# Kernel tuning notes

Measured on AMD Instinct MI355X. Metric: run time of the kernel, lower is better.

The kernel has to match this reference:

```python
import jax, jax.numpy as jnp
import numpy as np

N_NODES = 50000


def _gcn_conv(x, src, dst, W, b, num_nodes):
    """PyG GCNConv: out = D^{-1/2}(A+I)D^{-1/2} (x @ W) + b, self-loops added."""
    h = x @ W  # [N, out]
    # degrees over edges incl. self-loops (src/dst already include self-loops)
    ones = jnp.ones(src.shape[0], dtype=h.dtype)
    deg = jax.ops.segment_sum(ones, dst, num_segments=num_nodes)
    dinv = jnp.where(deg > 0, jax.lax.rsqrt(deg), 0.0)
    norm = dinv[src] * dinv[dst]  # [E]
    msgs = h[src] * norm[:, None]  # [E, out] gather (memory-bound)
    out = jax.ops.segment_sum(msgs, dst, num_segments=num_nodes)
    return out + b


def setup_inputs() -> dict:
    key = jax.random.key(0)
    ks = jax.random.split(key, 8)
    in_c, h2, h1, out_c = 256, 256, 128, 128
    x = jax.random.normal(ks[0], (N_NODES, in_c), dtype=jnp.float32)
    edge_index = jax.random.randint(ks[1], (2, 800000), 0, N_NODES, dtype=jnp.int64)
    def glorot(k, fi, fo):
        s = float(np.sqrt(6.0 / (fi + fo)))
        return jax.random.uniform(k, (fi, fo), jnp.float32, -s, s)
    return {
        "x": x,
        "edge_index": edge_index,
        "W1": glorot(ks[2], in_c, h2), "b1": jnp.zeros((h2,), jnp.float32),
        "W2": glorot(ks[3], h2, h1), "b2": jnp.zeros((h1,), jnp.float32),
        "W3": glorot(ks[4], h1, out_c), "b3": jnp.zeros((out_c,), jnp.float32),
    }


def reference(x, edge_index, W1, b1, W2, b2, W3, b3):
    n = x.shape[0]
    loops = jnp.arange(n, dtype=edge_index.dtype)
    src = jnp.concatenate([edge_index[0], loops])
    dst = jnp.concatenate([edge_index[1], loops])
    # dropout is a no-op in eval mode (training=False)
    h1 = jax.nn.relu(_gcn_conv(x, src, dst, W1, b1, n))
    h2 = jax.nn.relu(_gcn_conv(h1, src, dst, W2, b2, n))
    h3 = jax.nn.relu(_gcn_conv(h2, src, dst, W3, b3, n))
    return jnp.concatenate([h1, h2, h3], axis=1)
```

## Files before the change

kernel.cpp:

```cpp
#include <hip/hip_runtime.h>

typedef __attribute__((ext_vector_type(8))) short bfrag8;
typedef __attribute__((ext_vector_type(4))) float f32x4v;

__device__ inline short f2bf(float f) {
    unsigned u = __builtin_bit_cast(unsigned, f);
    u = (u + 0x7FFFu + ((u >> 16) & 1u)) >> 16;
    return (short)u;
}
__device__ inline float bf2f(short s) {
    unsigned u = ((unsigned)(unsigned short)s) << 16;
    return __builtin_bit_cast(float, u);
}
__device__ inline int pack2(short lo, short hi) {
    return (int)(((unsigned)(unsigned short)lo) | (((unsigned)(unsigned short)hi) << 16));
}
__device__ inline int pad16i(int v) { return (v + 15) & ~15; }


__global__ void deg_count_kernel(const int* __restrict__ dst, int E, int* __restrict__ deg) {
    int e = blockIdx.x * blockDim.x + threadIdx.x;
    if (e < E) atomicAdd(&deg[dst[e]], 1);
}

__global__ void block_sum_kernel(const int* __restrict__ deg, int n, int* __restrict__ bsums) {
    int i = blockIdx.x * 256 + threadIdx.x;
    int v = (i < n) ? pad16i(deg[i] + 1) : 0;
#pragma unroll
    for (int off = 32; off > 0; off >>= 1) v += __shfl_down(v, off);
    __shared__ int wsum[4];
    int lane = threadIdx.x & 63, w = threadIdx.x >> 6;
    if (lane == 0) wsum[w] = v;
    __syncthreads();
    if (threadIdx.x == 0) bsums[blockIdx.x] = wsum[0] + wsum[1] + wsum[2] + wsum[3];
}

__global__ void scan_bsums_kernel(int* __restrict__ bsums, int B, int* __restrict__ offs, int n) {
    __shared__ int s[256];
    int tid = threadIdx.x;
    int v = (tid < B) ? bsums[tid] : 0;
    s[tid] = v;
    __syncthreads();
    for (int off = 1; off < 256; off <<= 1) {
        int t = (tid >= off) ? s[tid - off] : 0;
        __syncthreads();
        s[tid] += t;
        __syncthreads();
    }
    if (tid < B) bsums[tid] = (tid == 0) ? 0 : s[tid - 1];
    if (tid == 0) offs[n] = s[255];
}

__global__ void scan_final_kernel(const int* __restrict__ deg, int n,
                                  const int* __restrict__ bsums,
                                  int* __restrict__ offs, int* __restrict__ cursor,
                                  float* __restrict__ dinv, int* __restrict__ csr) {
    __shared__ int s[256];
    int tid = threadIdx.x;
    int i = blockIdx.x * 256 + tid;
    int vt = (i < n) ? deg[i] + 1 : 0;
    int pv = (i < n) ? pad16i(vt) : 0;
    s[tid] = pv;
    __syncthreads();
    for (int off = 1; off < 256; off <<= 1) {
        int t = (tid >= off) ? s[tid - off] : 0;
        __syncthreads();
        s[tid] += t;
        __syncthreads();
    }
    if (i < n) {
        int excl = s[tid] - pv + bsums[blockIdx.x];
        offs[i] = excl;
        csr[excl] = i;
        cursor[i] = excl + 1;
        for (int p = excl + vt; p < excl + pv; ++p) csr[p] = n;
        dinv[i] = rsqrtf((float)vt);
    } else {
        dinv[i] = 0.f;
    }
}

__global__ void csr_fill_kernel(const int* __restrict__ src, const int* __restrict__ dst, int E,
                                int* __restrict__ cursor, int* __restrict__ csr) {
    int e = blockIdx.x * blockDim.x + threadIdx.x;
    if (e < E) {
        int d = dst[e];
        int p = atomicAdd(&cursor[d], 1);
        csr[p] = src[e];
    }
}


__global__ void prep_w_kernel(const float* __restrict__ W1, short* __restrict__ Wt1,
                              const float* __restrict__ W2, short* __restrict__ Wt2,
                              const float* __restrict__ W3, short* __restrict__ Wt3) {
    int i = blockIdx.x * blockDim.x + threadIdx.x;
    if (i < 65536) {
        int k = i >> 8, n = i & 255;
        Wt1[n * 256 + k] = f2bf(W1[i]);
    } else if (i < 65536 + 32768) {
        int j = i - 65536;
        int k = j >> 7, n = j & 127;
        Wt2[n * 256 + k] = f2bf(W2[j]);
    } else {
        int j = i - 65536 - 32768;
        int k = j >> 7, n = j & 127;
        Wt3[n * 128 + k] = f2bf(W3[j]);
    }
}


__global__ void x2b_kernel(const float* __restrict__ x, short* __restrict__ xb,
                           int total8, int totalp8) {
    int i = blockIdx.x * blockDim.x + threadIdx.x;
    if (i < total8) {
        const float4* p = (const float4*)(x + (size_t)i * 8);
        float4 v0 = p[0], v1 = p[1];
        int4 w = make_int4(pack2(f2bf(v0.x), f2bf(v0.y)), pack2(f2bf(v0.z), f2bf(v0.w)),
                           pack2(f2bf(v1.x), f2bf(v1.y)), pack2(f2bf(v1.z), f2bf(v1.w)));
        *(int4*)(xb + (size_t)i * 8) = w;
    } else if (i < totalp8) {
        *(int4*)(xb + (size_t)i * 8) = make_int4(0, 0, 0, 0);
    }
}


template<int K>
__global__ __launch_bounds__(256, 2) void gemm_skinny_kernel(
        const short* __restrict__ A,
        const short* __restrict__ Bt,
        const float* __restrict__ dinv,
        short* __restrict__ Tout, int ldt) {
    constexpr int BSTR = K + 8;
    __shared__ short Bs[64 * BSTR];

    const int tid = threadIdx.x;
    const int lane = tid & 63;
    const int wid = tid >> 6;
    const int l15 = lane & 15;
    const int quad = lane >> 4;
    const int q8 = quad * 8;
    const int bn = blockIdx.y * 64;
    const int row0 = blockIdx.x * 256 + wid * 64;

    {
        constexpr int TOT16 = 64 * K / 8;
#pragma unroll
        for (int i = tid; i < TOT16; i += 256) {
            int r = i / (K / 8);
            int c = (i % (K / 8)) * 8;
            *(int4*)&Bs[r * BSTR + c] = *(const int4*)&Bt[(size_t)(bn + r) * K + c];
        }
    }
    __syncthreads();

    f32x4v acc[4][4];
#pragma unroll
    for (int i = 0; i < 4; ++i)
#pragma unroll
        for (int j = 0; j < 4; ++j) acc[i][j] = (f32x4v){0.f, 0.f, 0.f, 0.f};

    const short* aBase = A + (size_t)(row0 + l15) * K + q8;

#pragma unroll
    for (int ks = 0; ks < K / 32; ++ks) {
        bfrag8 af[4], bf[4];
#pragma unroll
        for (int mt = 0; mt < 4; ++mt)
            af[mt] = *(const bfrag8*)(aBase + (size_t)mt * 16 * K + ks * 32);
#pragma unroll
        for (int nt = 0; nt < 4; ++nt)
            bf[nt] = *(const bfrag8*)&Bs[(nt * 16 + l15) * BSTR + ks * 32 + q8];
#pragma unroll
        for (int mt = 0; mt < 4; ++mt)
#pragma unroll
            for (int nt = 0; nt < 4; ++nt)
                acc[mt][nt] = __builtin_amdgcn_mfma_f32_16x16x32_bf16(af[mt], bf[nt], acc[mt][nt], 0, 0, 0);
    }

#pragma unroll
    for (int mt = 0; mt < 4; ++mt) {
#pragma unroll
        for (int r = 0; r < 4; ++r) {
            int grow = row0 + mt * 16 + quad * 4 + r;
            float di = dinv[grow];
            short* outp = Tout + (size_t)grow * ldt + bn + l15;
#pragma unroll
            for (int nt = 0; nt < 4; ++nt)
                outp[nt * 16] = f2bf(acc[mt][nt][r] * di);
        }
    }
}


template<bool WB>
__global__ __launch_bounds__(256) void agg256_kernel(
        const short* __restrict__ hn, const float* __restrict__ dinv,
        const int* __restrict__ offs, const int* __restrict__ csr,
        const float* __restrict__ bias, float* __restrict__ out,
        short* __restrict__ hb, int coloff, int n) {
    int node = blockIdx.x * 4 + (threadIdx.x >> 6);
    if (node >= n) return;
    int lane = threadIdx.x & 63;
    int hl = lane & 31;
    int sub = lane >> 5;
    const short* base = hn + hl * 8;

    float acc[8];
#pragma unroll
    for (int v = 0; v < 8; ++v) acc[v] = 0.f;

    int beg = offs[node], end = offs[node + 1];
    for (int e = beg + sub; e < end; e += 16) {
        int s[8];
#pragma unroll
        for (int j = 0; j < 8; ++j) s[j] = csr[e + 2 * j];
        bfrag8 r[8];
#pragma unroll
        for (int j = 0; j < 8; ++j) r[j] = *(const bfrag8*)(base + (size_t)s[j] * 256);
#pragma unroll
        for (int j = 0; j < 8; ++j)
#pragma unroll
            for (int v = 0; v < 8; ++v) acc[v] += bf2f(r[j][v]);
    }

#pragma unroll
    for (int v = 0; v < 8; ++v) acc[v] += __shfl_xor(acc[v], 32);

    if (sub == 0) {
        float di = dinv[node];
        float res[8];
#pragma unroll
        for (int v = 0; v < 8; ++v)
            res[v] = fmaxf(fmaf(di, acc[v], bias[hl * 8 + v]), 0.f);
        float4* op = (float4*)(out + (size_t)node * 512 + coloff + hl * 8);
        op[0] = make_float4(res[0], res[1], res[2], res[3]);
        op[1] = make_float4(res[4], res[5], res[6], res[7]);
        if (WB) {
            int4 w = make_int4(pack2(f2bf(res[0]), f2bf(res[1])), pack2(f2bf(res[2]), f2bf(res[3])),
                               pack2(f2bf(res[4]), f2bf(res[5])), pack2(f2bf(res[6]), f2bf(res[7])));
            *(int4*)(hb + (size_t)node * 256 + hl * 8) = w;
        }
    }
}


template<bool WB>
__global__ __launch_bounds__(256) void agg128_kernel(
        const short* __restrict__ hn, const float* __restrict__ dinv,
        const int* __restrict__ offs, const int* __restrict__ csr,
        const float* __restrict__ bias, float* __restrict__ out,
        short* __restrict__ hb, int coloff, int n) {
    int node = blockIdx.x * 4 + (threadIdx.x >> 6);
    if (node >= n) return;
    int lane = threadIdx.x & 63;
    int ch = lane & 15;
    int sub = lane >> 4;
    const short* base = hn + ch * 8;

    float acc[8];
#pragma unroll
    for (int v = 0; v < 8; ++v) acc[v] = 0.f;

    int beg = offs[node], end = offs[node + 1];
    int e = beg + sub;
    for (; e + 16 < end; e += 32) {
        int s[8];
#pragma unroll
        for (int j = 0; j < 8; ++j) s[j] = csr[e + 4 * j];
        bfrag8 r[8];
#pragma unroll
        for (int j = 0; j < 8; ++j) r[j] = *(const bfrag8*)(base + (size_t)s[j] * 128);
#pragma unroll
        for (int j = 0; j < 8; ++j)
#pragma unroll
            for (int v = 0; v < 8; ++v) acc[v] += bf2f(r[j][v]);
    }
    if (e < end) {
        int s[4];
#pragma unroll
        for (int j = 0; j < 4; ++j) s[j] = csr[e + 4 * j];
        bfrag8 r[4];
#pragma unroll
        for (int j = 0; j < 4; ++j) r[j] = *(const bfrag8*)(base + (size_t)s[j] * 128);
#pragma unroll
        for (int j = 0; j < 4; ++j)
#pragma unroll
            for (int v = 0; v < 8; ++v) acc[v] += bf2f(r[j][v]);
    }

#pragma unroll
    for (int v = 0; v < 8; ++v) {
        acc[v] += __shfl_xor(acc[v], 16);
        acc[v] += __shfl_xor(acc[v], 32);
    }

    if (sub == 0) {
        float di = dinv[node];
        float res[8];
#pragma unroll
        for (int v = 0; v < 8; ++v)
            res[v] = fmaxf(fmaf(di, acc[v], bias[ch * 8 + v]), 0.f);
        float4* op = (float4*)(out + (size_t)node * 512 + coloff + ch * 8);
        op[0] = make_float4(res[0], res[1], res[2], res[3]);
        op[1] = make_float4(res[4], res[5], res[6], res[7]);
        if (WB) {
            int4 w = make_int4(pack2(f2bf(res[0]), f2bf(res[1])), pack2(f2bf(res[2]), f2bf(res[3])),
                               pack2(f2bf(res[4]), f2bf(res[5])), pack2(f2bf(res[6]), f2bf(res[7])));
            *(int4*)(hb + (size_t)node * 128 + ch * 8) = w;
        }
    }
}


extern "C" void kernel_launch(void* const* d_in, const int* in_sizes, int n_in,
                              void* d_out, int out_size, void* d_ws, size_t ws_size,
                              hipStream_t stream) {
    const float* x  = (const float*)d_in[0];
    const int*   ei = (const int*)d_in[1];
    const float* W1 = (const float*)d_in[2];
    const float* b1 = (const float*)d_in[3];
    const float* W2 = (const float*)d_in[4];
    const float* b2 = (const float*)d_in[5];
    const float* W3 = (const float*)d_in[6];
    const float* b3 = (const float*)d_in[7];

    const int IN_C = 256, H2 = 256, H1 = 128, OUT_C = 128;
    int n = in_sizes[0] / IN_C;
    int E = in_sizes[1] / 2;
    const int* src = ei;
    const int* dst = ei + E;

    int sb = (n + 255) / 256;
    int npad = sb * 256;

    char* ws = (char*)d_ws;
    auto carve = [&](size_t bytes) { char* p = ws; ws += (bytes + 255) & ~(size_t)255; return p; };
    int*   deg    = (int*)  carve((size_t)n * 4);
    int*   offs   = (int*)  carve(((size_t)n + 1) * 4);
    int*   cursor = (int*)  carve((size_t)n * 4);
    float* dinv   = (float*)carve((size_t)npad * 4);
    int*   csr    = (int*)  carve(((size_t)E + 16 * (size_t)n) * 4);
    int*   bsums  = (int*)  carve(256 * 4);
    short* Wt1    = (short*)carve((size_t)IN_C * H2 * 2);
    short* Wt2    = (short*)carve((size_t)H2 * H1 * 2);
    short* Wt3    = (short*)carve((size_t)H1 * OUT_C * 2);
    short* t      = (short*)carve((size_t)npad * 256 * 2);
    short* inb    = (short*)carve((size_t)npad * 256 * 2);

    float* out = (float*)d_out;
    int nblk = (n + 255) / 256;

    hipMemsetAsync(deg, 0, (size_t)n * sizeof(int), stream);
    deg_count_kernel<<<(E + 255) / 256, 256, 0, stream>>>(dst, E, deg);
    block_sum_kernel<<<nblk, 256, 0, stream>>>(deg, n, bsums);
    scan_bsums_kernel<<<1, 256, 0, stream>>>(bsums, nblk, offs, n);
    scan_final_kernel<<<nblk, 256, 0, stream>>>(deg, n, bsums, offs, cursor, dinv, csr);
    csr_fill_kernel<<<(E + 255) / 256, 256, 0, stream>>>(src, dst, E, cursor, csr);

    prep_w_kernel<<<(65536 + 32768 + 16384 + 255) / 256, 256, 0, stream>>>(W1, Wt1, W2, Wt2, W3, Wt3);

    int total8 = n * IN_C / 8;
    int totalp8 = npad * IN_C / 8;
    x2b_kernel<<<(totalp8 + 255) / 256, 256, 0, stream>>>(x, inb, total8, totalp8);

    gemm_skinny_kernel<256><<<dim3(sb, H2 / 64), 256, 0, stream>>>(inb, Wt1, dinv, t, H2);
    agg256_kernel<true><<<(n + 3) / 4, 256, 0, stream>>>(t, dinv, offs, csr, b1, out, inb, 0, n);

    gemm_skinny_kernel<256><<<dim3(sb, H1 / 64), 256, 0, stream>>>(inb, Wt2, dinv, t, H1);
    agg128_kernel<true><<<(n + 3) / 4, 256, 0, stream>>>(t, dinv, offs, csr, b2, out, inb, H2, n);

    hipMemsetAsync(inb + (size_t)n * 128, 0, (size_t)(npad - n) * 128 * 2, stream);

    gemm_skinny_kernel<128><<<dim3(sb, OUT_C / 64), 256, 0, stream>>>(inb, Wt3, dinv, t, OUT_C);
    agg128_kernel<false><<<(n + 3) / 4, 256, 0, stream>>>(t, dinv, offs, csr, b3, out, nullptr, H2 + H1, n);
}
```

Before: 419.3 us.

## Widen GEMM N-tile with swizzled LDS, fuse prep kernels, pad CSR to 32

The skinny GEMM now computes a 128-column N tile per block (8 MFMA column tiles per wave) and stores B in LDS with an XOR swizzle instead of row padding. This halves the number of A-matrix reads across blocks. The weight and input bf16 conversion kernels are merged into one launch to save launch overhead. CSR rows are padded to multiples of 32, which removes the tail branch in agg128 at the cost of more padding gathers. The new GEMM tile raises register pressure (128 accumulators), and the removed dinv zeroing for padded rows may leave garbage in dinv for rows at or beyond n.

```diff
diff --git a/kernel.cpp b/kernel.cpp
--- a/kernel.cpp
+++ b/kernel.cpp
@@ -15,7 +15,7 @@
 __device__ inline int pack2(short lo, short hi) {
     return (int)(((unsigned)(unsigned short)lo) | (((unsigned)(unsigned short)hi) << 16));
 }
-__device__ inline int pad16i(int v) { return (v + 15) & ~15; }
+__device__ inline int pad32i(int v) { return (v + 31) & ~31; }
 
 
 __global__ void deg_count_kernel(const int* __restrict__ dst, int E, int* __restrict__ deg) {
@@ -25,7 +25,7 @@
 
 __global__ void block_sum_kernel(const int* __restrict__ deg, int n, int* __restrict__ bsums) {
     int i = blockIdx.x * 256 + threadIdx.x;
-    int v = (i < n) ? pad16i(deg[i] + 1) : 0;
+    int v = (i < n) ? pad32i(deg[i] + 1) : 0;
 #pragma unroll
     for (int off = 32; off > 0; off >>= 1) v += __shfl_down(v, off);
     __shared__ int wsum[4];
@@ -59,7 +59,7 @@
     int tid = threadIdx.x;
     int i = blockIdx.x * 256 + tid;
     int vt = (i < n) ? deg[i] + 1 : 0;
-    int pv = (i < n) ? pad16i(vt) : 0;
+    int pv = (i < n) ? pad32i(vt) : 0;
     s[tid] = pv;
     __syncthreads();
     for (int off = 1; off < 256; off <<= 1) {
@@ -75,8 +75,6 @@
         cursor[i] = excl + 1;
         for (int p = excl + vt; p < excl + pv; ++p) csr[p] = n;
         dinv[i] = rsqrtf((float)vt);
-    } else {
-        dinv[i] = 0.f;
     }
 }
 
@@ -91,27 +89,11 @@
 }
 
 
-__global__ void prep_w_kernel(const float* __restrict__ W1, short* __restrict__ Wt1,
-                              const float* __restrict__ W2, short* __restrict__ Wt2,
-                              const float* __restrict__ W3, short* __restrict__ Wt3) {
-    int i = blockIdx.x * blockDim.x + threadIdx.x;
-    if (i < 65536) {
-        int k = i >> 8, n = i & 255;
-        Wt1[n * 256 + k] = f2bf(W1[i]);
-    } else if (i < 65536 + 32768) {
-        int j = i - 65536;
-        int k = j >> 7, n = j & 127;
-        Wt2[n * 256 + k] = f2bf(W2[j]);
-    } else {
-        int j = i - 65536 - 32768;
-        int k = j >> 7, n = j & 127;
-        Wt3[n * 128 + k] = f2bf(W3[j]);
-    }
-}
-
-
-__global__ void x2b_kernel(const float* __restrict__ x, short* __restrict__ xb,
-                           int total8, int totalp8) {
+__global__ void prep_kernel(const float* __restrict__ x, short* __restrict__ xb,
+                            int total8, int totalp8,
+                            const float* __restrict__ W1, short* __restrict__ Wt1,
+                            const float* __restrict__ W2, short* __restrict__ Wt2,
+                            const float* __restrict__ W3, short* __restrict__ Wt3) {
     int i = blockIdx.x * blockDim.x + threadIdx.x;
     if (i < total8) {
         const float4* p = (const float4*)(x + (size_t)i * 8);
@@ -121,6 +103,20 @@
         *(int4*)(xb + (size_t)i * 8) = w;
     } else if (i < totalp8) {
         *(int4*)(xb + (size_t)i * 8) = make_int4(0, 0, 0, 0);
+    } else {
+        int j = i - totalp8;
+        if (j < 65536) {
+            int k = j >> 8, c = j & 255;
+            Wt1[c * 256 + k] = f2bf(W1[j]);
+        } else if (j < 65536 + 32768) {
+            int m = j - 65536;
+            int k = m >> 7, c = m & 127;
+            Wt2[c * 256 + k] = f2bf(W2[m]);
+        } else if (j < 65536 + 32768 + 16384) {
+            int m = j - 65536 - 32768;
+            int k = m >> 7, c = m & 127;
+            Wt3[c * 128 + k] = f2bf(W3[m]);
+        }
     }
 }
 
@@ -131,8 +127,8 @@
         const short* __restrict__ Bt,
         const float* __restrict__ dinv,
         short* __restrict__ Tout, int ldt) {
-    constexpr int BSTR = K + 8;
-    __shared__ short Bs[64 * BSTR];
+    __shared__ short Bs[128 * K];
+    char* bsb = (char*)Bs;
 
     const int tid = threadIdx.x;
     const int lane = tid & 63;
@@ -140,41 +136,47 @@
     const int l15 = lane & 15;
     const int quad = lane >> 4;
     const int q8 = quad * 8;
-    const int bn = blockIdx.y * 64;
+    const int bn = blockIdx.y * 128;
     const int row0 = blockIdx.x * 256 + wid * 64;
 
     {
-        constexpr int TOT16 = 64 * K / 8;
+        constexpr int TOT16 = 128 * K / 8;
 #pragma unroll
         for (int i = tid; i < TOT16; i += 256) {
             int r = i / (K / 8);
             int c = (i % (K / 8)) * 8;
-            *(int4*)&Bs[r * BSTR + c] = *(const int4*)&Bt[(size_t)(bn + r) * K + c];
+            int byte = (r * K + c) * 2;
+            byte ^= (r & 7) << 4;
+            *(int4*)(bsb + byte) = *(const int4*)&Bt[(size_t)(bn + r) * K + c];
         }
     }
     __syncthreads();
 
-    f32x4v acc[4][4];
+    f32x4v acc[4][8];
 #pragma unroll
     for (int i = 0; i < 4; ++i)
 #pragma unroll
-        for (int j = 0; j < 4; ++j) acc[i][j] = (f32x4v){0.f, 0.f, 0.f, 0.f};
+        for (int j = 0; j < 8; ++j) acc[i][j] = (f32x4v){0.f, 0.f, 0.f, 0.f};
 
     const short* aBase = A + (size_t)(row0 + l15) * K + q8;
 
 #pragma unroll
     for (int ks = 0; ks < K / 32; ++ks) {
-        bfrag8 af[4], bf[4];
+        bfrag8 af[4], bf[8];
 #pragma unroll
         for (int mt = 0; mt < 4; ++mt)
             af[mt] = *(const bfrag8*)(aBase + (size_t)mt * 16 * K + ks * 32);
 #pragma unroll
-        for (int nt = 0; nt < 4; ++nt)
-            bf[nt] = *(const bfrag8*)&Bs[(nt * 16 + l15) * BSTR + ks * 32 + q8];
+        for (int nt = 0; nt < 8; ++nt) {
+            int r = nt * 16 + l15;
+            int byte = (r * K + ks * 32 + q8) * 2;
+            byte ^= (r & 7) << 4;
+            bf[nt] = *(const bfrag8*)(bsb + byte);
+        }
 #pragma unroll
         for (int mt = 0; mt < 4; ++mt)
 #pragma unroll
-            for (int nt = 0; nt < 4; ++nt)
+            for (int nt = 0; nt < 8; ++nt)
                 acc[mt][nt] = __builtin_amdgcn_mfma_f32_16x16x32_bf16(af[mt], bf[nt], acc[mt][nt], 0, 0, 0);
     }
 
@@ -186,7 +188,7 @@
             float di = dinv[grow];
             short* outp = Tout + (size_t)grow * ldt + bn + l15;
 #pragma unroll
-            for (int nt = 0; nt < 4; ++nt)
+            for (int nt = 0; nt < 8; ++nt)
                 outp[nt * 16] = f2bf(acc[mt][nt][r] * di);
         }
     }
@@ -263,8 +265,7 @@
     for (int v = 0; v < 8; ++v) acc[v] = 0.f;
 
     int beg = offs[node], end = offs[node + 1];
-    int e = beg + sub;
-    for (; e + 16 < end; e += 32) {
+    for (int e = beg + sub; e < end; e += 32) {
         int s[8];
 #pragma unroll
         for (int j = 0; j < 8; ++j) s[j] = csr[e + 4 * j];
@@ -273,18 +274,6 @@
         for (int j = 0; j < 8; ++j) r[j] = *(const bfrag8*)(base + (size_t)s[j] * 128);
 #pragma unroll
         for (int j = 0; j < 8; ++j)
-#pragma unroll
-            for (int v = 0; v < 8; ++v) acc[v] += bf2f(r[j][v]);
-    }
-    if (e < end) {
-        int s[4];
-#pragma unroll
-        for (int j = 0; j < 4; ++j) s[j] = csr[e + 4 * j];
-        bfrag8 r[4];
-#pragma unroll
-        for (int j = 0; j < 4; ++j) r[j] = *(const bfrag8*)(base + (size_t)s[j] * 128);
-#pragma unroll
-        for (int j = 0; j < 4; ++j)
 #pragma unroll
             for (int v = 0; v < 8; ++v) acc[v] += bf2f(r[j][v]);
     }
@@ -340,7 +329,7 @@
     int*   offs   = (int*)  carve(((size_t)n + 1) * 4);
     int*   cursor = (int*)  carve((size_t)n * 4);
     float* dinv   = (float*)carve((size_t)npad * 4);
-    int*   csr    = (int*)  carve(((size_t)E + 16 * (size_t)n) * 4);
+    int*   csr    = (int*)  carve(((size_t)E + 32 * (size_t)n) * 4);
     int*   bsums  = (int*)  carve(256 * 4);
     short* Wt1    = (short*)carve((size_t)IN_C * H2 * 2);
     short* Wt2    = (short*)carve((size_t)H2 * H1 * 2);
@@ -358,20 +347,20 @@
     scan_final_kernel<<<nblk, 256, 0, stream>>>(deg, n, bsums, offs, cursor, dinv, csr);
     csr_fill_kernel<<<(E + 255) / 256, 256, 0, stream>>>(src, dst, E, cursor, csr);
 
-    prep_w_kernel<<<(65536 + 32768 + 16384 + 255) / 256, 256, 0, stream>>>(W1, Wt1, W2, Wt2, W3, Wt3);
-
     int total8 = n * IN_C / 8;
     int totalp8 = npad * IN_C / 8;
-    x2b_kernel<<<(totalp8 + 255) / 256, 256, 0, stream>>>(x, inb, total8, totalp8);
-
-    gemm_skinny_kernel<256><<<dim3(sb, H2 / 64), 256, 0, stream>>>(inb, Wt1, dinv, t, H2);
+    int prepTot = totalp8 + 65536 + 32768 + 16384;
+    prep_kernel<<<(prepTot + 255) / 256, 256, 0, stream>>>(
+        x, inb, total8, totalp8, W1, Wt1, W2, Wt2, W3, Wt3);
+
+    gemm_skinny_kernel<256><<<dim3(sb, H2 / 128), 256, 0, stream>>>(inb, Wt1, dinv, t, H2);
     agg256_kernel<true><<<(n + 3) / 4, 256, 0, stream>>>(t, dinv, offs, csr, b1, out, inb, 0, n);
 
-    gemm_skinny_kernel<256><<<dim3(sb, H1 / 64), 256, 0, stream>>>(inb, Wt2, dinv, t, H1);
+    gemm_skinny_kernel<256><<<dim3(sb, H1 / 128), 256, 0, stream>>>(inb, Wt2, dinv, t, H1);
     agg128_kernel<true><<<(n + 3) / 4, 256, 0, stream>>>(t, dinv, offs, csr, b2, out, inb, H2, n);
 
     hipMemsetAsync(inb + (size_t)n * 128, 0, (size_t)(npad - n) * 128 * 2, stream);
 
-    gemm_skinny_kernel<128><<<dim3(sb, OUT_C / 64), 256, 0, stream>>>(inb, Wt3, dinv, t, OUT_C);
+    gemm_skinny_kernel<128><<<dim3(sb, OUT_C / 128), 256, 0, stream>>>(inb, Wt3, dinv, t, OUT_C);
     agg128_kernel<false><<<(n + 3) / 4, 256, 0, stream>>>(t, dinv, offs, csr, b3, out, nullptr, H2 + H1, n);
 }
```

New measurement: 425.5 us. About the same (+1.5%).
